# Optimization experiments

Hardware: AMD Instinct MI355X
Metric: run time of the kernel (lower is better)

The kernel has to match this reference:

```python
import jax, jax.numpy as jnp
import numpy as np

WIN = 11
SIGMA = 1.5
C1 = 0.01 ** 2
C2 = 0.03 ** 2

def _gaussian_window(channel):
    x = np.arange(WIN)
    g = np.exp(-((x - WIN // 2) ** 2) / (2.0 * SIGMA ** 2))
    g = g / g.sum()
    w2d = np.outer(g, g).astype(np.float32)  # [11,11]
    # depthwise kernel: [C, 1, 11, 11] in OIHW with feature_group_count=C
    return jnp.asarray(np.broadcast_to(w2d, (channel, 1, WIN, WIN)).copy())

def _dwconv(x, w, channel):
    pad = WIN // 2
    return jax.lax.conv_general_dilated(
        x, w, window_strides=(1, 1), padding=[(pad, pad), (pad, pad)],
        dimension_numbers=('NCHW', 'OIHW', 'NCHW'),
        feature_group_count=channel)

def _ssim(img1, img2, window, channel):
    mu1 = _dwconv(img1, window, channel)
    mu2 = _dwconv(img2, window, channel)
    mu1_sq = mu1 * mu1
    mu2_sq = mu2 * mu2
    mu1_mu2 = mu1 * mu2
    sigma1_sq = _dwconv(img1 * img1, window, channel) - mu1_sq
    sigma2_sq = _dwconv(img2 * img2, window, channel) - mu2_sq
    sigma12 = _dwconv(img1 * img2, window, channel) - mu1_mu2
    ssim_map = ((2 * mu1_mu2 + C1) * (2 * sigma12 + C2)) / (
        (mu1_sq + mu2_sq + C1) * (sigma1_sq + sigma2_sq + C2))
    return ssim_map.mean()

def setup_inputs() -> dict:
    key = jax.random.key(0)
    kA, kB, kF = jax.random.split(key, 3)
    shape = (16, 3, 512, 512)
    return {
        'image_A': jax.random.uniform(kA, shape, dtype=jnp.float32),
        'image_B': jax.random.uniform(kB, shape, dtype=jnp.float32),
        'image_fused': jax.random.uniform(kF, shape, dtype=jnp.float32),
    }

def reference(image_A, image_B, image_fused):
    channel = image_A.shape[1]
    window = _gaussian_window(channel).astype(image_A.dtype)
    loss = 0.5 * _ssim(image_A, image_fused, window, channel) \
         + 0.5 * _ssim(image_B, image_fused, window, channel)
    return loss
```

## Files before the change

### kernel.cpp

```cpp
#include <hip/hip_runtime.h>
#include <math.h>

#define IMG_W 512
#define IMG_H 512
#define NPLANES 48
#define RROWS 32
#define NCHUNK 16
#define NSTRIP 8
#define WPB 4
#define NGROUP (NCHUNK / WPB)
#define NBLOCKS (NPLANES * NSTRIP * NGROUP)
#define SSIM_C1 1e-4f
#define SSIM_C2 9e-4f

typedef float f32x2 __attribute__((ext_vector_type(2)));

struct GW { float g[11]; };

__device__ __forceinline__ f32x2 splat2(float v) { return (f32x2){v, v}; }
__device__ __forceinline__ f32x2 fma2(f32x2 a, f32x2 b, f32x2 c) {
  return __builtin_elementwise_fma(a, b, c);
}

__device__ __forceinline__ float fdiv_fast(float n, float d) {
  float r = __builtin_amdgcn_rcpf(d);
  r = r * fmaf(-d, r, 2.0f);
  float q = n * r;
  q = fmaf(fmaf(-d, q, n), r, q);
  return q;
}

__global__ __launch_bounds__(256, 2) void ssim_main(
    const float* __restrict__ A, const float* __restrict__ B,
    const float* __restrict__ F, double* __restrict__ partials, GW gw)
{
  __shared__ float sA[WPB][2][2][80], sB[WPB][2][2][80], sF[WPB][2][2][80];
  __shared__ double sred[WPB];
  const int b = blockIdx.x;
  const int plane = b / (NSTRIP * NGROUP);
  const int rem   = b % (NSTRIP * NGROUP);
  const int strip = rem / NGROUP;
  const int grp   = rem % NGROUP;
  const int wid = threadIdx.x >> 6;
  const int t   = threadIdx.x & 63;
  const int chunk = grp * WPB + wid;
  const int x0 = strip * 64;
  const int y0 = chunk * RROWS;
  const size_t pbase = (size_t)plane * (IMG_W * IMG_H);
  const float* Ap = A + pbase;
  const float* Bp = B + pbase;
  const float* Fp = F + pbase;

  float (&mA)[2][2][80] = sA[wid];
  float (&mB)[2][2][80] = sB[wid];
  float (&mF)[2][2][80] = sF[wid];

  const int c  = x0 - 5 + t;
  const bool cok = (c >= 0) && (c < IMG_W);
  const int c2 = c + 64;
  const bool c2ok = (t < 10) && (c2 < IMG_W);

  f32x2 ring[7][6];
  #pragma unroll
  for (int s = 0; s < 7; ++s)
    #pragma unroll
    for (int k = 0; k < 6; ++k) ring[s][k] = splat2(0.f);

  float acc = 0.f;

  float rA0,rB0,rF0,xA0,xB0,xF0, rA1,rB1,rF1,xA1,xB1,xF1;
  auto load_pair = [&](int ii) {
    const int yin0 = y0 - 5 + 2*ii;
    const int yin1 = yin0 + 1;
    const bool r0 = (yin0 >= 0) && (yin0 < IMG_H);
    const bool r1 = (yin1 >= 0) && (yin1 < IMG_H);
    const size_t o0 = (size_t)yin0 * IMG_W;
    const size_t o1 = (size_t)yin1 * IMG_W;
    rA0 = (r0 && cok) ? Ap[o0 + c] : 0.f;
    rB0 = (r0 && cok) ? Bp[o0 + c] : 0.f;
    rF0 = (r0 && cok) ? Fp[o0 + c] : 0.f;
    rA1 = (r1 && cok) ? Ap[o1 + c] : 0.f;
    rB1 = (r1 && cok) ? Bp[o1 + c] : 0.f;
    rF1 = (r1 && cok) ? Fp[o1 + c] : 0.f;
    xA0 = (r0 && c2ok) ? Ap[o0 + c2] : 0.f;
    xB0 = (r0 && c2ok) ? Bp[o0 + c2] : 0.f;
    xF0 = (r0 && c2ok) ? Fp[o0 + c2] : 0.f;
    xA1 = (r1 && c2ok) ? Ap[o1 + c2] : 0.f;
    xB1 = (r1 && c2ok) ? Bp[o1 + c2] : 0.f;
    xF1 = (r1 && c2ok) ? Fp[o1 + c2] : 0.f;
  };

  load_pair(0);

  for (int jj = 0; jj < 4; ++jj) {
    #pragma unroll
    for (int ph = 0; ph < 6; ++ph) {
      const int ii = jj * 6 + ph;
      if (ii < 21) {
        const int buf = ii & 1;
        mA[buf][0][t] = rA0; mA[buf][1][t] = rA1;
        mB[buf][0][t] = rB0; mB[buf][1][t] = rB1;
        mF[buf][0][t] = rF0; mF[buf][1][t] = rF1;
        if (t < 10) {
          mA[buf][0][t+64] = xA0; mA[buf][1][t+64] = xA1;
          mB[buf][0][t+64] = xB0; mB[buf][1][t+64] = xB1;
          mF[buf][0][t+64] = xF0; mF[buf][1][t+64] = xF1;
        }
        if (ii < 20) load_pair(ii + 1);
        f32x2 hA=splat2(0.f), hB=splat2(0.f), hF=splat2(0.f),
              hA2=splat2(0.f), hB2=splat2(0.f), hF2=splat2(0.f),
              hAF=splat2(0.f), hBF=splat2(0.f);
        #pragma unroll
        for (int k = 0; k < 11; ++k) {
          const float w = gw.g[k];
          const f32x2 a  = {mA[buf][0][t+k], mA[buf][1][t+k]};
          const f32x2 bb = {mB[buf][0][t+k], mB[buf][1][t+k]};
          const f32x2 f  = {mF[buf][0][t+k], mF[buf][1][t+k]};
          const f32x2 wv = splat2(w);
          const f32x2 wa = wv*a, wb = wv*bb, wf = wv*f;
          hA += wa; hB += wb; hF += wf;
          hA2 = fma2(wa, a, hA2); hB2 = fma2(wb, bb, hB2); hF2 = fma2(wf, f, hF2);
          hAF = fma2(wa, f, hAF); hBF = fma2(wb, f, hBF);
        }
        ring[0][ph]=hA;  ring[1][ph]=hB;  ring[2][ph]=hF;
        ring[3][ph]=hA2+hF2;  ring[4][ph]=hB2+hF2;
        ring[5][ph]=hAF; ring[6][ph]=hBF;

        if (ii >= 5) {
          f32x2 M[7];
          #pragma unroll
          for (int s = 0; s < 7; ++s) M[s] = splat2(0.f);
          #pragma unroll
          for (int k = 0; k < 11; ++k) {
            const float w = gw.g[k];
            const int plo = (ph + 1 + (k >> 1)) % 6;
            const int phi = (ph + 1 + ((k + 1) >> 1)) % 6;
            #pragma unroll
            for (int s = 0; s < 7; ++s) {
              const float elo = (k & 1)       ? ring[s][plo].y : ring[s][plo].x;
              const float ehi = ((k + 1) & 1) ? ring[s][phi].y : ring[s][phi].x;
              M[s].x = fmaf(w, elo, M[s].x);
              M[s].y = fmaf(w, ehi, M[s].y);
            }
          }
          const f32x2 mAv=M[0], mBv=M[1], mFv=M[2];
          const f32x2 vS1=M[3], vS2=M[4], vAF=M[5], vBF=M[6];
          const f32x2 mA2=mAv*mAv, mB2=mBv*mBv, mF2=mFv*mFv,
                      mAF=mAv*mFv, mBF=mBv*mFv;
          const f32x2 sAFv = vAF - mAF, sBFv = vBF - mBF;
          const f32x2 ts1 = vS1 - mA2 - mF2;
          const f32x2 ts2 = vS2 - mB2 - mF2;
          const f32x2 two = splat2(2.f), c1 = splat2(SSIM_C1), c2v = splat2(SSIM_C2);
          const f32x2 n1 = fma2(two, mAF, c1) * fma2(two, sAFv, c2v);
          const f32x2 d1 = (mA2 + mF2 + c1) * (ts1 + c2v);
          const f32x2 n2 = fma2(two, mBF, c1) * fma2(two, sBFv, c2v);
          const f32x2 d2 = (mB2 + mF2 + c1) * (ts2 + c2v);
          acc += fdiv_fast(n1.x, d1.x) + fdiv_fast(n2.x, d2.x);
          acc += fdiv_fast(n1.y, d1.y) + fdiv_fast(n2.y, d2.y);
        }
      }
    }
  }

  float wsum = acc;
  #pragma unroll
  for (int off = 32; off > 0; off >>= 1)
    wsum += __shfl_down(wsum, off, 64);
  if (t == 0) sred[wid] = (double)wsum;
  __syncthreads();
  if (threadIdx.x == 0)
    partials[b] = sred[0] + sred[1] + sred[2] + sred[3];
}

__global__ __launch_bounds__(256) void ssim_final(
    const double* __restrict__ partials, float* __restrict__ out)
{
  __shared__ double sd[256];
  const int t = threadIdx.x;
  double s = 0.0;
  for (int i = t; i < NBLOCKS; i += 256) s += partials[i];
  sd[t] = s;
  __syncthreads();
  for (int off = 128; off > 0; off >>= 1) {
    if (t < off) sd[t] += sd[t + off];
    __syncthreads();
  }
  if (t == 0)
    out[0] = (float)(0.5 * sd[0] / (double)(16.0 * 3.0 * 512.0 * 512.0));
}

extern "C" void kernel_launch(void* const* d_in, const int* in_sizes, int n_in,
                              void* d_out, int out_size, void* d_ws, size_t ws_size,
                              hipStream_t stream) {
  const float* A = (const float*)d_in[0];
  const float* B = (const float*)d_in[1];
  const float* F = (const float*)d_in[2];
  double* partials = (double*)d_ws;

  GW gw;
  double g[11], s = 0.0;
  for (int i = 0; i < 11; ++i) { g[i] = exp(-((double)((i-5)*(i-5))) / 4.5); s += g[i]; }
  for (int i = 0; i < 11; ++i) gw.g[i] = (float)(g[i] / s);

  hipLaunchKernelGGL(ssim_main, dim3(NBLOCKS), dim3(WPB * 64), 0, stream,
                     A, B, F, partials, gw);
  hipLaunchKernelGGL(ssim_final, dim3(1), dim3(256), 0, stream,
                     partials, (float*)d_out);
}
```

Baseline: 215.2 us.

## Interleave LDS rows into vector layout and pack vertical FMAs

Shared memory is reorganised so each column's two rows of A and B sit in one float4 and F's two rows in one float2. The horizontal pass now does two wide LDS reads per tap instead of six scalar ones. In the vertical pass, even taps use packed two-wide FMA on aligned ring pairs, while odd taps keep scalar FMAs for the cross-pair case. A compiler memory fence is added after the LDS stores; wider per-lane LDS accesses may change bank conflict behaviour.

```diff
diff --git a/kernel.cpp b/kernel.cpp
--- a/kernel.cpp
+++ b/kernel.cpp
@@ -14,6 +14,7 @@
 #define SSIM_C2 9e-4f
 
 typedef float f32x2 __attribute__((ext_vector_type(2)));
+typedef float f32x4 __attribute__((ext_vector_type(4)));
 
 struct GW { float g[11]; };
 
@@ -30,11 +31,14 @@
   return q;
 }
 
+#define LDS_ORDER_FENCE() asm volatile("" ::: "memory")
+
 __global__ __launch_bounds__(256, 2) void ssim_main(
     const float* __restrict__ A, const float* __restrict__ B,
     const float* __restrict__ F, double* __restrict__ partials, GW gw)
 {
-  __shared__ float sA[WPB][2][2][80], sB[WPB][2][2][80], sF[WPB][2][2][80];
+  __shared__ f32x4 sAB[WPB][2][80];
+  __shared__ f32x2 sFF[WPB][2][80];
   __shared__ double sred[WPB];
   const int b = blockIdx.x;
   const int plane = b / (NSTRIP * NGROUP);
@@ -51,9 +55,8 @@
   const float* Bp = B + pbase;
   const float* Fp = F + pbase;
 
-  float (&mA)[2][2][80] = sA[wid];
-  float (&mB)[2][2][80] = sB[wid];
-  float (&mF)[2][2][80] = sF[wid];
+  f32x4 (&mAB)[2][80] = sAB[wid];
+  f32x2 (&mFF)[2][80] = sFF[wid];
 
   const int c  = x0 - 5 + t;
   const bool cok = (c >= 0) && (c < IMG_W);
@@ -98,14 +101,13 @@
       const int ii = jj * 6 + ph;
       if (ii < 21) {
         const int buf = ii & 1;
-        mA[buf][0][t] = rA0; mA[buf][1][t] = rA1;
-        mB[buf][0][t] = rB0; mB[buf][1][t] = rB1;
-        mF[buf][0][t] = rF0; mF[buf][1][t] = rF1;
+        mAB[buf][t] = (f32x4){rA0, rA1, rB0, rB1};
+        mFF[buf][t] = (f32x2){rF0, rF1};
         if (t < 10) {
-          mA[buf][0][t+64] = xA0; mA[buf][1][t+64] = xA1;
-          mB[buf][0][t+64] = xB0; mB[buf][1][t+64] = xB1;
-          mF[buf][0][t+64] = xF0; mF[buf][1][t+64] = xF1;
+          mAB[buf][t+64] = (f32x4){xA0, xA1, xB0, xB1};
+          mFF[buf][t+64] = (f32x2){xF0, xF1};
         }
+        LDS_ORDER_FENCE();
         if (ii < 20) load_pair(ii + 1);
         f32x2 hA=splat2(0.f), hB=splat2(0.f), hF=splat2(0.f),
               hA2=splat2(0.f), hB2=splat2(0.f), hF2=splat2(0.f),
@@ -113,9 +115,10 @@
         #pragma unroll
         for (int k = 0; k < 11; ++k) {
           const float w = gw.g[k];
-          const f32x2 a  = {mA[buf][0][t+k], mA[buf][1][t+k]};
-          const f32x2 bb = {mB[buf][0][t+k], mB[buf][1][t+k]};
-          const f32x2 f  = {mF[buf][0][t+k], mF[buf][1][t+k]};
+          const f32x4 ab = mAB[buf][t+k];
+          const f32x2 f  = mFF[buf][t+k];
+          const f32x2 a  = {ab.x, ab.y};
+          const f32x2 bb = {ab.z, ab.w};
           const f32x2 wv = splat2(w);
           const f32x2 wa = wv*a, wb = wv*bb, wf = wv*f;
           hA += wa; hB += wb; hF += wf;
@@ -133,14 +136,19 @@
           #pragma unroll
           for (int k = 0; k < 11; ++k) {
             const float w = gw.g[k];
-            const int plo = (ph + 1 + (k >> 1)) % 6;
-            const int phi = (ph + 1 + ((k + 1) >> 1)) % 6;
-            #pragma unroll
-            for (int s = 0; s < 7; ++s) {
-              const float elo = (k & 1)       ? ring[s][plo].y : ring[s][plo].x;
-              const float ehi = ((k + 1) & 1) ? ring[s][phi].y : ring[s][phi].x;
-              M[s].x = fmaf(w, elo, M[s].x);
-              M[s].y = fmaf(w, ehi, M[s].y);
+            if ((k & 1) == 0) {
+              const int p = (ph + 1 + (k >> 1)) % 6;
+              const f32x2 wv = splat2(w);
+              #pragma unroll
+              for (int s = 0; s < 7; ++s) M[s] = fma2(wv, ring[s][p], M[s]);
+            } else {
+              const int plo = (ph + 1 + (k >> 1)) % 6;
+              const int phi = (plo + 1) % 6;
+              #pragma unroll
+              for (int s = 0; s < 7; ++s) {
+                M[s].x = fmaf(w, ring[s][plo].y, M[s].x);
+                M[s].y = fmaf(w, ring[s][phi].x, M[s].y);
+              }
             }
           }
           const f32x2 mAv=M[0], mBv=M[1], mFv=M[2];
```

New measurement: 207.5 us. 3.6% less time.
